# Kernel optimization log

Measured on AMD Instinct MI355X. Metric: run time of the kernel, lower is better.

Reference implementation:

```python
import jax, jax.numpy as jnp
import numpy as np

B, N, D = 256, 64, 256   # graphs, nodes/graph, hidden dim (node_size*extend_dim)
T, E = B * N, 524288     # total nodes, total edges
NODE, BOND, K = 128, 16, 3
RRELU_SLOPE = (1.0 / 8.0 + 1.0 / 3.0) / 2.0  # eval-mode RReLU slope


def rrelu(x):
    return jnp.where(x >= 0, x, RRELU_SLOPE * x)


def conv_step(x, src, dst, ea, Wn, We, bm, Ws, bs):
    # message on each edge, scatter-add to destination, self-transform + update
    msg = jax.nn.relu(x[src] @ Wn + ea @ We + bm)          # [E, D]
    agg = jax.ops.segment_sum(msg, dst, num_segments=T)    # [T, D]
    return jax.nn.relu(x @ Ws + agg + bs)


def readout(x):
    # GlobalPool: cat([mean, sum, sort_pool(k=3)], -1) -> [B, 5D]
    xr = x.reshape(B, N, D)
    mean, s = xr.mean(1), xr.sum(1)
    order = jnp.argsort(-xr[..., -1], axis=1)[:, :K]                      # [B, K]
    topk = jnp.take_along_axis(xr, order[..., None], axis=1).reshape(B, K * D)
    return jnp.concatenate([mean, s, topk], -1)


def dot_pool(x1, x2):
    # per-graph cross-molecule dot product, max & mean -> [B, 2]
    item = jnp.einsum('bnd,bmd->bnm', x1.reshape(B, N, D), x2.reshape(B, N, D))
    return jnp.stack([item.max((1, 2)), item.mean((1, 2))], -1)


def setup_inputs() -> dict:
    key = jax.random.key(0)
    ks = jax.random.split(key, 32)
    batch = jnp.repeat(jnp.arange(B, dtype=jnp.int64), N)
    off = jnp.repeat(jnp.arange(B, dtype=jnp.int64) * N, E // B)

    def edges(k):
        s = jax.random.randint(k, (2, E), 0, N).astype(jnp.int64) + off[None, :]
        return s

    def w(k, shape):
        fan = shape[0]
        return jax.random.normal(k, shape, jnp.float32) * (1.0 / np.sqrt(fan))

    return {
        'x1': jax.random.normal(ks[0], (T, NODE), jnp.float32),
        'edge_index1': edges(ks[1]),
        'edge_attr1': jax.random.normal(ks[2], (E, BOND), jnp.float32),
        'batch1': batch,
        'x2': jax.random.normal(ks[3], (T, NODE), jnp.float32),
        'edge_index2': edges(ks[4]),
        'edge_attr2': jax.random.normal(ks[5], (E, BOND), jnp.float32),
        'batch2': batch,
        'W0_1': w(ks[6], (NODE, D)), 'b0_1': jnp.zeros(D),
        'W0_2': w(ks[7], (NODE, D)), 'b0_2': jnp.zeros(D),
        'Wn1': w(ks[8], (D, D)), 'We1': w(ks[9], (BOND, D)), 'bm1': jnp.zeros(D),
        'Ws1': w(ks[10], (D, D)), 'bs1': jnp.zeros(D),
        'Wn2': w(ks[11], (D, D)), 'We2': w(ks[12], (BOND, D)), 'bm2': jnp.zeros(D),
        'Ws2': w(ks[13], (D, D)), 'bs2': jnp.zeros(D),
        'Wf1': w(ks[14], (5 * D, D)), 'bf1': jnp.zeros(D),
        'Wf2': w(ks[15], (5 * D, D)), 'bf2': jnp.zeros(D),
        'Wo1': w(ks[16], (2 * D + 6, D)), 'bo1': jnp.zeros(D),
        'Wo2': w(ks[17], (D, 2)), 'bo2': jnp.zeros(2),
    }


def reference(x1, edge_index1, edge_attr1, batch1, x2, edge_index2, edge_attr2, batch2,
              W0_1, b0_1, W0_2, b0_2,
              Wn1, We1, bm1, Ws1, bs1,
              Wn2, We2, bm2, Ws2, bs2,
              Wf1, bf1, Wf2, bf2, Wo1, bo1, Wo2, bo2):
    xm1 = rrelu(x1 @ W0_1 + b0_1)
    xm2 = rrelu(x2 @ W0_2 + b0_2)
    s1, d1 = edge_index1[0], edge_index1[1]
    s2, d2 = edge_index2[0], edge_index2[1]
    fusion = []
    for _ in range(3):  # message_steps
        xm1 = conv_step(xm1, s1, d1, edge_attr1, Wn1, We1, bm1, Ws1, bs1)
        xm2 = conv_step(xm2, s2, d2, edge_attr2, Wn2, We2, bm2, Ws2, bs2)
        fusion.append(dot_pool(xm1, xm2))
    outm1 = readout(xm1) @ Wf1 + bf1
    outm2 = readout(xm2) @ Wf2 + bf2
    out = jnp.concatenate([outm1, outm2, jnp.concatenate(fusion, -1)], -1)
    out = out @ Wo1 + bo1
    return out @ Wo2 + bo2
```

## Files before the change

kernel.cpp:

```cpp
#include <hip/hip_runtime.h>
#include <hip/hip_fp16.h>

#define E_TOTAL 524288
#define RRELU_SLOPE 0.22916666666666666f

typedef float f32x4 __attribute__((ext_vector_type(4)));
typedef short short8_t __attribute__((ext_vector_type(8)));
typedef _Float16 half4_t __attribute__((ext_vector_type(4)));
typedef _Float16 h2v __attribute__((ext_vector_type(2)));

#define MFMA16F16 __builtin_amdgcn_mfma_f32_16x16x16f16

#if defined(__HIP_DEVICE_COMPILE__)
# if __has_builtin(__builtin_amdgcn_cvt_pkrtz)
#  define HAVE_PKRTZ 1
# endif
#endif

__device__ inline unsigned short f2bf(float x) {
  unsigned int u = __float_as_uint(x);
  u += 0x7FFFu + ((u >> 16) & 1u);
  return (unsigned short)(u >> 16);
}

__device__ inline unsigned int pack_h2(float a, float b) {
  __half2 h = __floats2half2_rn(a, b);
  return __builtin_bit_cast(unsigned int, h);
}

__device__ inline unsigned int pack_h2_fast(float a, float b) {
#ifdef HAVE_PKRTZ
  return __builtin_bit_cast(unsigned int, __builtin_amdgcn_cvt_pkrtz(a, b));
#else
  return pack_h2(a, b);
#endif
}

__device__ inline float dot4(float4 a, float4 b) {
  return a.x * b.x + a.y * b.y + a.z * b.z + a.w * b.w;
}

__global__ __launch_bounds__(256) void gemm_bf16_dual(
    const float* __restrict__ A1, const unsigned short* __restrict__ BT1,
    const float* __restrict__ bias1, float* __restrict__ C1,
    const float* __restrict__ A2, const unsigned short* __restrict__ BT2,
    const float* __restrict__ bias2, float* __restrict__ C2,
    int lda, int ldc, int K, int act)
{
  const float* A = blockIdx.z ? A2 : A1;
  const unsigned short* BT = blockIdx.z ? BT2 : BT1;
  const float* bias = blockIdx.z ? bias2 : bias1;
  float* C = blockIdx.z ? C2 : C1;

  __shared__ unsigned short As[128][32];
  __shared__ unsigned short Bs[128][32];
  const int tid = threadIdx.x;
  const int bm = blockIdx.x, bn = blockIdx.y;
  const int w = tid >> 6, l = tid & 63;
  const int wm = (w & 1) * 64, wn = (w >> 1) * 64;
  const int q = l >> 4, r = l & 15;

  f32x4 acc[4][4];
  for (int i = 0; i < 4; ++i)
    for (int j = 0; j < 4; ++j)
      acc[i][j] = (f32x4){0.f, 0.f, 0.f, 0.f};

  const int sm = tid >> 1;
  const int sk = (tid & 1) * 16;
  const float* ap = A + (size_t)(bm * 128 + sm) * lda + sk;
  const unsigned short* bp = BT + (size_t)(bn * 128 + sm) * K + sk;

  for (int k0 = 0; k0 < K; k0 += 32) {
    float4 f0 = *(const float4*)(ap + k0);
    float4 f1 = *(const float4*)(ap + k0 + 4);
    float4 f2 = *(const float4*)(ap + k0 + 8);
    float4 f3 = *(const float4*)(ap + k0 + 12);
    uint4 p0, p1;
    p0.x = (unsigned)f2bf(f0.x) | ((unsigned)f2bf(f0.y) << 16);
    p0.y = (unsigned)f2bf(f0.z) | ((unsigned)f2bf(f0.w) << 16);
    p0.z = (unsigned)f2bf(f1.x) | ((unsigned)f2bf(f1.y) << 16);
    p0.w = (unsigned)f2bf(f1.z) | ((unsigned)f2bf(f1.w) << 16);
    p1.x = (unsigned)f2bf(f2.x) | ((unsigned)f2bf(f2.y) << 16);
    p1.y = (unsigned)f2bf(f2.z) | ((unsigned)f2bf(f2.w) << 16);
    p1.z = (unsigned)f2bf(f3.x) | ((unsigned)f2bf(f3.y) << 16);
    p1.w = (unsigned)f2bf(f3.z) | ((unsigned)f2bf(f3.w) << 16);
    *(uint4*)&As[sm][sk] = p0;
    *(uint4*)&As[sm][sk + 8] = p1;
    uint4 b0 = *(const uint4*)(bp + k0);
    uint4 b1 = *(const uint4*)(bp + k0 + 8);
    *(uint4*)&Bs[sm][sk] = b0;
    *(uint4*)&Bs[sm][sk + 8] = b1;
    __syncthreads();

    short8_t af[4], bfr[4];
    for (int mt = 0; mt < 4; ++mt)
      af[mt] = *(const short8_t*)&As[wm + mt * 16 + r][q * 8];
    for (int nt = 0; nt < 4; ++nt)
      bfr[nt] = *(const short8_t*)&Bs[wn + nt * 16 + r][q * 8];
    for (int mt = 0; mt < 4; ++mt)
      for (int nt = 0; nt < 4; ++nt)
        acc[mt][nt] = __builtin_amdgcn_mfma_f32_16x16x32_bf16(
            af[mt], bfr[nt], acc[mt][nt], 0, 0, 0);
    __syncthreads();
  }

  for (int nt = 0; nt < 4; ++nt) {
    int gc = bn * 128 + wn + nt * 16 + r;
    float bv = bias ? bias[gc] : 0.f;
    for (int mt = 0; mt < 4; ++mt) {
      int gm = bm * 128 + wm + mt * 16 + q * 4;
      for (int rr = 0; rr < 4; ++rr) {
        float v = acc[mt][nt][rr] + bv;
        if (act == 2) v = (v >= 0.f) ? v : v * RRELU_SLOPE;
        C[(size_t)(gm + rr) * ldc + gc] = v;
      }
    }
  }
}

__global__ __launch_bounds__(256) void sort_edges_dual(
    const int* __restrict__ ei1, const int* __restrict__ ei2,
    int* __restrict__ meta1, int* __restrict__ meta2,
    int* __restrict__ perm1, int* __restrict__ perm2,
    int* __restrict__ starts1, int* __restrict__ starts2)
{
  const int mol = blockIdx.x >> 8;
  const int g = blockIdx.x & 255;
  const int* eidx = mol ? ei2 : ei1;
  int* meta = mol ? meta2 : meta1;
  int* perm = mol ? perm2 : perm1;
  int* starts = mol ? starts2 : starts1;

  __shared__ int cnt[4][64];
  __shared__ int startS[65];
  __shared__ int cur[64];
  const int t = threadIdx.x, w = t >> 6;
  cnt[w][t & 63] = 0;
  if (t < 64) cur[t] = 0;
  __syncthreads();
  for (int i = t; i < 2048; i += 256)
    atomicAdd(&cnt[w][eidx[E_TOTAL + g * 2048 + i] & 63], 1);
  __syncthreads();
  if (t == 0) {
    int acc = 0;
    for (int n = 0; n < 64; ++n) {
      startS[n] = acc;
      acc += cnt[0][n] + cnt[1][n] + cnt[2][n] + cnt[3][n];
    }
    startS[64] = acc;
  }
  __syncthreads();
  if (t < 65) starts[g * 65 + t] = startS[t];
  for (int i = t; i < 2048; i += 256) {
    int s = eidx[g * 2048 + i] & 63;
    int d = eidx[E_TOTAL + g * 2048 + i] & 63;
    int p = startS[d] + atomicAdd(&cur[d], 1);
    meta[g * 2048 + p] = s | (d << 8);
    perm[g * 2048 + p] = i;
  }
}

__global__ __launch_bounds__(256) void ea_gather_pack_dual(
    const float* __restrict__ ea1, const float* __restrict__ ea2,
    const int* __restrict__ perm1, const int* __restrict__ perm2,
    unsigned int* __restrict__ o1, unsigned int* __restrict__ o2)
{
  const int mol = blockIdx.x >> 11;
  const float* ea = mol ? ea2 : ea1;
  const int* perm = mol ? perm2 : perm1;
  unsigned int* out = mol ? o2 : o1;
  int p = (blockIdx.x & 2047) * 256 + threadIdx.x;
  int g = p >> 11;
  int i = perm[p];
  const float* s = ea + (size_t)(g * 2048 + i) * 16;
  float4 v0 = *(const float4*)(s);
  float4 v1 = *(const float4*)(s + 4);
  float4 v2 = *(const float4*)(s + 8);
  float4 v3 = *(const float4*)(s + 12);
  uint4 q0, q1;
  q0.x = pack_h2(v0.x, v0.y); q0.y = pack_h2(v0.z, v0.w);
  q0.z = pack_h2(v1.x, v1.y); q0.w = pack_h2(v1.z, v1.w);
  q1.x = pack_h2(v2.x, v2.y); q1.y = pack_h2(v2.z, v2.w);
  q1.z = pack_h2(v3.x, v3.y); q1.w = pack_h2(v3.z, v3.w);
  *(uint4*)(out + (size_t)p * 8) = q0;
  *(uint4*)(out + (size_t)p * 8 + 4) = q1;
}

__global__ __launch_bounds__(512, 4) void edge_conv_dual(
    const float* __restrict__ y1, const int* __restrict__ meta1,
    const unsigned int* __restrict__ eas1, const unsigned int* __restrict__ wep1,
    const int* __restrict__ st1, float* __restrict__ xo1,
    const float* __restrict__ y2, const int* __restrict__ meta2,
    const unsigned int* __restrict__ eas2, const unsigned int* __restrict__ wep2,
    const int* __restrict__ st2, float* __restrict__ xo2)
{
  const float* y; const int* meta; const unsigned int* eas;
  const unsigned int* wep; const int* st; float* xo;
  if (blockIdx.z == 0) { y = y1; meta = meta1; eas = eas1; wep = wep1; st = st1; xo = xo1; }
  else                 { y = y2; meta = meta2; eas = eas2; wep = wep2; st = st2; xo = xo2; }

  __shared__ unsigned int ypk[4160];
  const int g = blockIdx.x >> 1;
  const int dbase = (blockIdx.x & 1) * 128;
  const int tid = threadIdx.x;
  const int l = tid & 63;
  const int w = tid >> 6;
  const int rh = l & 15;
  const int qh = l >> 4;
  const int rhw = w * 8 + rh;

  for (int i = tid; i < 4096; i += 512) {
    int n = i >> 6, j = i & 63;
    const float* yr = y + (size_t)(g * 64 + n) * 512 + dbase + j;
    ypk[n * 65 + j] = pack_h2_fast(yr[0], yr[64]);
  }

  uint2 bfr[8];
#pragma unroll
  for (int c = 0; c < 8; ++c) {
    int d = dbase + c * 16 + rh;
    bfr[c].x = wep[(2 * qh) * 256 + d];
    bfr[c].y = wep[(2 * qh + 1) * 256 + d];
  }

  __syncthreads();

  const int estart = st[g * 65 + w * 8];
  const int eend   = st[g * 65 + w * 8 + 8];

  f32x4 acc[8];
#pragma unroll
  for (int i = 0; i < 8; ++i) acc[i] = (f32x4){0.f, 0.f, 0.f, 0.f};

  int base = estart;
  uint2 af = {0u, 0u};
  int mv = -1;
  if (base < eend) {
    int lim = eend - base; if (lim > 16) lim = 16;
    af = *(const uint2*)(eas + ((size_t)g * 2048 + base + (rh < lim ? rh : lim - 1)) * 8 + 2 * qh);
    int m = meta[(size_t)g * 2048 + base + (l < lim ? l : lim - 1)];
    mv = (l < lim) ? m : -1;
  }

  while (base < eend) {
    int mp[4];
#pragma unroll
    for (int v = 0; v < 4; ++v)
      mp[v] = __builtin_amdgcn_ds_bpermute(qh * 16 + v * 4, mv);

    int nbase = base + 16;
    uint2 afn = af;
    int mvn = -1;
    if (nbase < eend) {
      int nlim = eend - nbase; if (nlim > 16) nlim = 16;
      afn = *(const uint2*)(eas + ((size_t)g * 2048 + nbase + (rh < nlim ? rh : nlim - 1)) * 8 + 2 * qh);
      int m2 = meta[(size_t)g * 2048 + nbase + (l < nlim ? l : nlim - 1)];
      mvn = (l < nlim) ? m2 : -1;
    }

    half4_t afh = __builtin_bit_cast(half4_t, af);
    f32x4 pa[4], pb[4];
#pragma unroll
    for (int cp = 0; cp < 4; ++cp) {
      f32x4 z = (f32x4){0.f, 0.f, 0.f, 0.f};
      pa[cp] = MFMA16F16(afh, __builtin_bit_cast(half4_t, bfr[cp]), z, 0, 0, 0);
      pb[cp] = MFMA16F16(afh, __builtin_bit_cast(half4_t, bfr[cp + 4]), z, 0, 0, 0);
    }

    unsigned int yv[4][4];
    unsigned int ind[4];
#pragma unroll
    for (int v = 0; v < 4; ++v) {
      int sv = mp[v] & 63;
      int dv = (mp[v] >> 8) & 255;
      const unsigned int* yb = ypk + sv * 65 + rh;
      yv[0][v] = yb[0];
      yv[1][v] = yb[16];
      yv[2][v] = yb[32];
      yv[3][v] = yb[48];
      ind[v] = (dv == rhw) ? 0x3C00u : 0u;
    }
    uint2 su;
    su.x = ind[0] | (ind[1] << 16);
    su.y = ind[2] | (ind[3] << 16);
    half4_t sfrag = __builtin_bit_cast(half4_t, su);

    const h2v hz = {(_Float16)0.0f, (_Float16)0.0f};
#pragma unroll
    for (int cp = 0; cp < 4; ++cp) {
      unsigned int t[4];
#pragma unroll
      for (int v = 0; v < 4; ++v) {
        h2v s = __builtin_bit_cast(h2v, pack_h2_fast(pa[cp][v], pb[cp][v]));
        s = s + __builtin_bit_cast(h2v, yv[cp][v]);
        s = __builtin_elementwise_max(s, hz);
        t[v] = __builtin_bit_cast(unsigned int, s);
      }
      uint2 blo, bhi;
      blo.x = __builtin_amdgcn_perm(t[1], t[0], 0x05040100u);
      blo.y = __builtin_amdgcn_perm(t[3], t[2], 0x05040100u);
      bhi.x = __builtin_amdgcn_perm(t[1], t[0], 0x07060302u);
      bhi.y = __builtin_amdgcn_perm(t[3], t[2], 0x07060302u);
      acc[cp]     = MFMA16F16(sfrag, __builtin_bit_cast(half4_t, blo), acc[cp], 0, 0, 0);
      acc[cp + 4] = MFMA16F16(sfrag, __builtin_bit_cast(half4_t, bhi), acc[cp + 4], 0, 0, 0);
    }

    base = nbase;
    af = afn;
    mv = mvn;
  }

  if (qh < 2) {
#pragma unroll
    for (int v = 0; v < 4; ++v) {
      int node = g * 64 + w * 8 + qh * 4 + v;
      const float* ysp = y + (size_t)node * 512 + 256 + dbase + rh;
      float* xop = xo + (size_t)node * 256 + dbase + rh;
#pragma unroll
      for (int cp = 0; cp < 8; ++cp) {
        int dim = (cp & 3) * 16 + (cp >> 2) * 64;
        xop[dim] = fmaxf(ysp[dim] + acc[cp][v], 0.f);
      }
    }
  }
}

__global__ __launch_bounds__(256) void dot_pool_k(
    const float* __restrict__ x1, const float* __restrict__ x2,
    float* __restrict__ fusion, int step)
{
  __shared__ float s1[64][68];
  __shared__ float s2[64][68];
  __shared__ float redm[4], reds[4];
  const int g = blockIdx.x;
  const int tid = threadIdx.x;
  const int ti = (tid & 15) * 4;
  const int tj = (tid >> 4) * 4;
  float acc[4][4] = {};
  for (int kc = 0; kc < 256; kc += 64) {
    for (int rr = 0; rr < 4; ++rr) {
      int lin = tid + rr * 256;
      int n = lin >> 4, k4 = (lin & 15) * 4;
      *(float4*)&s1[n][k4] = *(const float4*)(x1 + (size_t)(g * 64 + n) * 256 + kc + k4);
      *(float4*)&s2[n][k4] = *(const float4*)(x2 + (size_t)(g * 64 + n) * 256 + kc + k4);
    }
    __syncthreads();
    for (int kk = 0; kk < 64; kk += 4) {
      float4 a0 = *(const float4*)&s1[ti + 0][kk];
      float4 a1 = *(const float4*)&s1[ti + 1][kk];
      float4 a2 = *(const float4*)&s1[ti + 2][kk];
      float4 a3 = *(const float4*)&s1[ti + 3][kk];
      float4 b0 = *(const float4*)&s2[tj + 0][kk];
      float4 b1 = *(const float4*)&s2[tj + 1][kk];
      float4 b2 = *(const float4*)&s2[tj + 2][kk];
      float4 b3 = *(const float4*)&s2[tj + 3][kk];
      acc[0][0] += dot4(a0, b0); acc[0][1] += dot4(a0, b1);
      acc[0][2] += dot4(a0, b2); acc[0][3] += dot4(a0, b3);
      acc[1][0] += dot4(a1, b0); acc[1][1] += dot4(a1, b1);
      acc[1][2] += dot4(a1, b2); acc[1][3] += dot4(a1, b3);
      acc[2][0] += dot4(a2, b0); acc[2][1] += dot4(a2, b1);
      acc[2][2] += dot4(a2, b2); acc[2][3] += dot4(a2, b3);
      acc[3][0] += dot4(a3, b0); acc[3][1] += dot4(a3, b1);
      acc[3][2] += dot4(a3, b2); acc[3][3] += dot4(a3, b3);
    }
    __syncthreads();
  }
  float mymax = -1e30f, mysum = 0.f;
  for (int i = 0; i < 4; ++i)
    for (int j = 0; j < 4; ++j) {
      mymax = fmaxf(mymax, acc[i][j]);
      mysum += acc[i][j];
    }
  for (int off = 32; off; off >>= 1) {
    mymax = fmaxf(mymax, __shfl_down(mymax, off, 64));
    mysum += __shfl_down(mysum, off, 64);
  }
  if ((tid & 63) == 0) { redm[tid >> 6] = mymax; reds[tid >> 6] = mysum; }
  __syncthreads();
  if (tid == 0) {
    float gm = fmaxf(fmaxf(redm[0], redm[1]), fmaxf(redm[2], redm[3]));
    float gs = reds[0] + reds[1] + reds[2] + reds[3];
    fusion[g * 6 + step * 2] = gm;
    fusion[g * 6 + step * 2 + 1] = gs * (1.f / 4096.f);
  }
}

__global__ __launch_bounds__(256) void readout_dual(
    const float* __restrict__ xm1, const float* __restrict__ xm2,
    float* __restrict__ R1, float* __restrict__ R2)
{
  const int mol = blockIdx.x >> 8;
  const float* xm = mol ? xm2 : xm1;
  float* R = mol ? R2 : R1;
  __shared__ float lastcol[64];
  __shared__ int topi[3];
  const int g = blockIdx.x & 255, d = threadIdx.x;
  float s = 0.f;
  for (int n = 0; n < 64; ++n) s += xm[(size_t)(g * 64 + n) * 256 + d];
  R[(size_t)g * 1280 + d] = s * (1.f / 64.f);
  R[(size_t)g * 1280 + 256 + d] = s;
  if (d < 64) lastcol[d] = xm[(size_t)(g * 64 + d) * 256 + 255];
  __syncthreads();
  if (d == 0) {
    unsigned long long used = 0;
    for (int j = 0; j < 3; ++j) {
      float best = -1e30f;
      int bi = 0;
      for (int n = 0; n < 64; ++n) {
        if ((used >> n) & 1ull) continue;
        if (lastcol[n] > best) { best = lastcol[n]; bi = n; }
      }
      used |= (1ull << bi);
      topi[j] = bi;
    }
  }
  __syncthreads();
  for (int j = 0; j < 3; ++j)
    R[(size_t)g * 1280 + 512 + j * 256 + d] =
        xm[(size_t)(g * 64 + topi[j]) * 256 + d];
}

__global__ __launch_bounds__(256) void final_head(
    const float* __restrict__ outm1, const float* __restrict__ outm2,
    const float* __restrict__ fusion,
    const float* __restrict__ Wo1, const float* __restrict__ bo1,
    const float* __restrict__ Wo2, const float* __restrict__ bo2,
    float* __restrict__ out)
{
  __shared__ float cat[520];
  __shared__ float r0s[4], r1s[4];
  const int g = blockIdx.x, t = threadIdx.x;
  cat[t] = outm1[(size_t)g * 256 + t];
  cat[256 + t] = outm2[(size_t)g * 256 + t];
  if (t < 6) cat[512 + t] = fusion[g * 6 + t];
  __syncthreads();
  float a0 = 0.f, a1 = 0.f, a2 = 0.f, a3 = 0.f;
  for (int k = 0; k < 516; k += 4) {
    a0 = fmaf(cat[k],     Wo1[(size_t)(k)     * 256 + t], a0);
    a1 = fmaf(cat[k + 1], Wo1[(size_t)(k + 1) * 256 + t], a1);
    a2 = fmaf(cat[k + 2], Wo1[(size_t)(k + 2) * 256 + t], a2);
    a3 = fmaf(cat[k + 3], Wo1[(size_t)(k + 3) * 256 + t], a3);
  }
  a0 = fmaf(cat[516], Wo1[(size_t)516 * 256 + t], a0);
  a1 = fmaf(cat[517], Wo1[(size_t)517 * 256 + t], a1);
  float acc = bo1[t] + ((a0 + a1) + (a2 + a3));
  float p0 = acc * Wo2[t * 2];
  float p1 = acc * Wo2[t * 2 + 1];
  for (int off = 32; off; off >>= 1) {
    p0 += __shfl_down(p0, off, 64);
    p1 += __shfl_down(p1, off, 64);
  }
  if ((t & 63) == 0) { r0s[t >> 6] = p0; r1s[t >> 6] = p1; }
  __syncthreads();
  if (t == 0) {
    out[g * 2] = r0s[0] + r0s[1] + r0s[2] + r0s[3] + bo2[0];
    out[g * 2 + 1] = r1s[0] + r1s[1] + r1s[2] + r1s[3] + bo2[1];
  }
}

__global__ __launch_bounds__(256) void transpose_all(
    const float* __restrict__ W0_1, const float* __restrict__ W0_2,
    const float* __restrict__ Wn1, const float* __restrict__ Ws1,
    const float* __restrict__ Wn2, const float* __restrict__ Ws2,
    const float* __restrict__ Wf1, const float* __restrict__ Wf2,
    unsigned short* __restrict__ W0T1, unsigned short* __restrict__ W0T2,
    unsigned short* __restrict__ WcT1, unsigned short* __restrict__ WcT2,
    unsigned short* __restrict__ WfT1, unsigned short* __restrict__ WfT2)
{
  const int b = blockIdx.x, n = threadIdx.x;
  const float* src;
  unsigned short* dst;
  int k, K;
  if (b < 128)       { src = W0_1; dst = W0T1;        k = b;        K = 128; }
  else if (b < 256)  { src = W0_2; dst = W0T2;        k = b - 128;  K = 128; }
  else if (b < 512)  { src = Wn1;  dst = WcT1;        k = b - 256;  K = 256; }
  else if (b < 768)  { src = Ws1;  dst = WcT1 + 65536;k = b - 512;  K = 256; }
  else if (b < 1024) { src = Wn2;  dst = WcT2;        k = b - 768;  K = 256; }
  else if (b < 1280) { src = Ws2;  dst = WcT2 + 65536;k = b - 1024; K = 256; }
  else if (b < 2560) { src = Wf1;  dst = WfT1;        k = b - 1280; K = 1280; }
  else               { src = Wf2;  dst = WfT2;        k = b - 2560; K = 1280; }
  dst[n * K + k] = f2bf(src[(size_t)k * 256 + n]);
}

__global__ void misc_prep(
    const float* bm1, const float* bs1, const float* bm2, const float* bs2,
    const float* We1, const float* We2,
    float* bcat1, float* bcat2,
    unsigned int* weh1, unsigned int* weh2)
{
  int idx = blockIdx.x * 256 + threadIdx.x;
  if (idx < 512) {
    bcat1[idx] = idx < 256 ? bm1[idx] : bs1[idx - 256];
  } else if (idx < 1024) {
    int i = idx - 512;
    bcat2[i] = i < 256 ? bm2[i] : bs2[i - 256];
  } else if (idx < 3072) {
    int i = idx - 1024, j = i >> 8, d = i & 255;
    weh1[i] = pack_h2(We1[(2 * j) * 256 + d], We1[(2 * j + 1) * 256 + d]);
  } else if (idx < 5120) {
    int i = idx - 3072, j = i >> 8, d = i & 255;
    weh2[i] = pack_h2(We2[(2 * j) * 256 + d], We2[(2 * j + 1) * 256 + d]);
  }
}

extern "C" void kernel_launch(void* const* d_in, const int* in_sizes, int n_in,
                              void* d_out, int out_size, void* d_ws, size_t ws_size,
                              hipStream_t stream)
{
  const float* x1 = (const float*)d_in[0];
  const int* ei1 = (const int*)d_in[1];
  const float* ea1 = (const float*)d_in[2];
  const float* x2 = (const float*)d_in[4];
  const int* ei2 = (const int*)d_in[5];
  const float* ea2 = (const float*)d_in[6];
  const float* W0_1 = (const float*)d_in[8];
  const float* b0_1 = (const float*)d_in[9];
  const float* W0_2 = (const float*)d_in[10];
  const float* b0_2 = (const float*)d_in[11];
  const float* Wn1 = (const float*)d_in[12];
  const float* We1 = (const float*)d_in[13];
  const float* bm1 = (const float*)d_in[14];
  const float* Ws1 = (const float*)d_in[15];
  const float* bs1 = (const float*)d_in[16];
  const float* Wn2 = (const float*)d_in[17];
  const float* We2 = (const float*)d_in[18];
  const float* bm2 = (const float*)d_in[19];
  const float* Ws2 = (const float*)d_in[20];
  const float* bs2 = (const float*)d_in[21];
  const float* Wf1 = (const float*)d_in[22];
  const float* bf1 = (const float*)d_in[23];
  const float* Wf2 = (const float*)d_in[24];
  const float* bf2 = (const float*)d_in[25];
  const float* Wo1 = (const float*)d_in[26];
  const float* bo1 = (const float*)d_in[27];
  const float* Wo2 = (const float*)d_in[28];
  const float* bo2 = (const float*)d_in[29];
  float* out = (float*)d_out;

  float* w = (float*)d_ws;
  size_t off = 0;
  auto alloc = [&](size_t nf) { float* p = w + off; off += nf; return p; };
  float* xmA1 = alloc(4194304);
  float* xmA2 = alloc(4194304);
  float* xmB1 = alloc(4194304);
  float* xmB2 = alloc(4194304);
  float* y1 = alloc(8388608);
  float* y2 = alloc(8388608);
  float* R1 = alloc(327680);
  float* R2 = alloc(327680);
  float* outm1 = alloc(65536);
  float* outm2 = alloc(65536);
  float* fusion = alloc(1536);
  float* bcat1 = alloc(512);
  float* bcat2 = alloc(512);
  unsigned short* W0T1 = (unsigned short*)alloc(16384);
  unsigned short* W0T2 = (unsigned short*)alloc(16384);
  unsigned short* WcT1 = (unsigned short*)alloc(65536);
  unsigned short* WcT2 = (unsigned short*)alloc(65536);
  unsigned short* WfT1 = (unsigned short*)alloc(163840);
  unsigned short* WfT2 = (unsigned short*)alloc(163840);
  unsigned int* weh1 = (unsigned int*)alloc(2048);
  unsigned int* weh2 = (unsigned int*)alloc(2048);
  unsigned int* eah1 = (unsigned int*)alloc(4194304);
  unsigned int* eah2 = (unsigned int*)alloc(4194304);
  int* meta1 = (int*)alloc(524288);
  int* meta2 = (int*)alloc(524288);
  int* perm1 = (int*)alloc(524288);
  int* perm2 = (int*)alloc(524288);
  int* starts1 = (int*)alloc(16640);
  int* starts2 = (int*)alloc(16640);
  (void)in_sizes; (void)n_in; (void)out_size; (void)ws_size;

  sort_edges_dual<<<512, 256, 0, stream>>>(ei1, ei2, meta1, meta2,
                                           perm1, perm2, starts1, starts2);
  transpose_all<<<3840, 256, 0, stream>>>(W0_1, W0_2, Wn1, Ws1, Wn2, Ws2,
                                          Wf1, Wf2, W0T1, W0T2, WcT1, WcT2,
                                          WfT1, WfT2);
  misc_prep<<<20, 256, 0, stream>>>(bm1, bs1, bm2, bs2, We1, We2,
                                    bcat1, bcat2, weh1, weh2);
  ea_gather_pack_dual<<<4096, 256, 0, stream>>>(ea1, ea2, perm1, perm2,
                                                eah1, eah2);

  gemm_bf16_dual<<<dim3(128, 2, 2), 256, 0, stream>>>(
      x1, W0T1, b0_1, xmA1, x2, W0T2, b0_2, xmA2, 128, 256, 128, 2);

  float* cur1 = xmA1; float* cur2 = xmA2;
  float* nxt1 = xmB1; float* nxt2 = xmB2;
  for (int step = 0; step < 3; ++step) {
    gemm_bf16_dual<<<dim3(128, 4, 2), 256, 0, stream>>>(
        cur1, WcT1, bcat1, y1, cur2, WcT2, bcat2, y2, 256, 512, 256, 0);
    edge_conv_dual<<<dim3(512, 1, 2), 512, 0, stream>>>(
        y1, meta1, eah1, weh1, starts1, nxt1,
        y2, meta2, eah2, weh2, starts2, nxt2);
    dot_pool_k<<<256, 256, 0, stream>>>(nxt1, nxt2, fusion, step);
    float* t1 = cur1; cur1 = nxt1; nxt1 = t1;
    float* t2 = cur2; cur2 = nxt2; nxt2 = t2;
  }

  readout_dual<<<512, 256, 0, stream>>>(cur1, cur2, R1, R2);
  gemm_bf16_dual<<<dim3(2, 2, 2), 256, 0, stream>>>(
      R1, WfT1, bf1, outm1, R2, WfT2, bf2, outm2, 1280, 256, 1280, 0);
  final_head<<<256, 256, 0, stream>>>(outm1, outm2, fusion,
                                      Wo1, bo1, Wo2, bo2, out);
}
```

Measured before the change: 593.5 us.

## Emit bf16 node features for conv GEMM and MFMA dot-pool, tile weight transpose

The edge convolution and the initial projection now also write a bf16 copy of the node features. A new GEMM variant reads that bf16 copy directly instead of converting fp32 A tiles on load. The dot-pool kernel is rewritten to use bf16 MFMA with XOR-swizzled shared memory in place of the fp32 scalar dot products. The weight transpose now goes through a shared-memory tile with vectorized stores. This cuts A-operand bandwidth and moves dot-pool onto the matrix cores, at the cost of extra bf16 writes from edge_conv and lower precision in the dot-pool max and mean.

```diff
diff --git a/kernel.cpp b/kernel.cpp
--- a/kernel.cpp
+++ b/kernel.cpp
@@ -36,21 +36,20 @@
 #endif
 }
 
-__device__ inline float dot4(float4 a, float4 b) {
-  return a.x * b.x + a.y * b.y + a.z * b.z + a.w * b.w;
-}
-
 __global__ __launch_bounds__(256) void gemm_bf16_dual(
     const float* __restrict__ A1, const unsigned short* __restrict__ BT1,
     const float* __restrict__ bias1, float* __restrict__ C1,
+    unsigned short* __restrict__ Ch1,
     const float* __restrict__ A2, const unsigned short* __restrict__ BT2,
     const float* __restrict__ bias2, float* __restrict__ C2,
+    unsigned short* __restrict__ Ch2,
     int lda, int ldc, int K, int act)
 {
   const float* A = blockIdx.z ? A2 : A1;
   const unsigned short* BT = blockIdx.z ? BT2 : BT1;
   const float* bias = blockIdx.z ? bias2 : bias1;
   float* C = blockIdx.z ? C2 : C1;
+  unsigned short* Ch = blockIdx.z ? Ch2 : Ch1;
 
   __shared__ unsigned short As[128][32];
   __shared__ unsigned short Bs[128][32];
@@ -112,8 +111,73 @@
       for (int rr = 0; rr < 4; ++rr) {
         float v = acc[mt][nt][rr] + bv;
         if (act == 2) v = (v >= 0.f) ? v : v * RRELU_SLOPE;
-        C[(size_t)(gm + rr) * ldc + gc] = v;
+        if (Ch) Ch[(size_t)(gm + rr) * ldc + gc] = f2bf(v);
+        else    C[(size_t)(gm + rr) * ldc + gc] = v;
       }
+    }
+  }
+}
+
+__global__ __launch_bounds__(256) void gemm_h_dual(
+    const unsigned short* __restrict__ Ah1, const unsigned short* __restrict__ BT1,
+    const float* __restrict__ bias1, float* __restrict__ C1,
+    const unsigned short* __restrict__ Ah2, const unsigned short* __restrict__ BT2,
+    const float* __restrict__ bias2, float* __restrict__ C2,
+    int ldc, int K)
+{
+  const unsigned short* A = blockIdx.z ? Ah2 : Ah1;
+  const unsigned short* BT = blockIdx.z ? BT2 : BT1;
+  const float* bias = blockIdx.z ? bias2 : bias1;
+  float* C = blockIdx.z ? C2 : C1;
+
+  __shared__ unsigned short As[128][32];
+  __shared__ unsigned short Bs[128][32];
+  const int tid = threadIdx.x;
+  const int bm = blockIdx.x, bn = blockIdx.y;
+  const int w = tid >> 6, l = tid & 63;
+  const int wm = (w & 1) * 64, wn = (w >> 1) * 64;
+  const int q = l >> 4, r = l & 15;
+
+  f32x4 acc[4][4];
+  for (int i = 0; i < 4; ++i)
+    for (int j = 0; j < 4; ++j)
+      acc[i][j] = (f32x4){0.f, 0.f, 0.f, 0.f};
+
+  const int sm = tid >> 1;
+  const int sk = (tid & 1) * 16;
+  const unsigned short* ap = A + (size_t)(bm * 128 + sm) * K + sk;
+  const unsigned short* bp = BT + (size_t)(bn * 128 + sm) * K + sk;
+
+  for (int k0 = 0; k0 < K; k0 += 32) {
+    uint4 a0 = *(const uint4*)(ap + k0);
+    uint4 a1 = *(const uint4*)(ap + k0 + 8);
+    uint4 b0 = *(const uint4*)(bp + k0);
+    uint4 b1 = *(const uint4*)(bp + k0 + 8);
+    *(uint4*)&As[sm][sk] = a0;
+    *(uint4*)&As[sm][sk + 8] = a1;
+    *(uint4*)&Bs[sm][sk] = b0;
+    *(uint4*)&Bs[sm][sk + 8] = b1;
+    __syncthreads();
+
+    short8_t af[4], bfr[4];
+    for (int mt = 0; mt < 4; ++mt)
+      af[mt] = *(const short8_t*)&As[wm + mt * 16 + r][q * 8];
+    for (int nt = 0; nt < 4; ++nt)
+      bfr[nt] = *(const short8_t*)&Bs[wn + nt * 16 + r][q * 8];
+    for (int mt = 0; mt < 4; ++mt)
+      for (int nt = 0; nt < 4; ++nt)
+        acc[mt][nt] = __builtin_amdgcn_mfma_f32_16x16x32_bf16(
+            af[mt], bfr[nt], acc[mt][nt], 0, 0, 0);
+    __syncthreads();
+  }
+
+  for (int nt = 0; nt < 4; ++nt) {
+    int gc = bn * 128 + wn + nt * 16 + r;
+    float bv = bias ? bias[gc] : 0.f;
+    for (int mt = 0; mt < 4; ++mt) {
+      int gm = bm * 128 + wm + mt * 16 + q * 4;
+      for (int rr = 0; rr < 4; ++rr)
+        C[(size_t)(gm + rr) * ldc + gc] = acc[mt][nt][rr] + bv;
     }
   }
 }
@@ -190,14 +254,16 @@
     const float* __restrict__ y1, const int* __restrict__ meta1,
     const unsigned int* __restrict__ eas1, const unsigned int* __restrict__ wep1,
     const int* __restrict__ st1, float* __restrict__ xo1,
+    unsigned short* __restrict__ xoh1,
     const float* __restrict__ y2, const int* __restrict__ meta2,
     const unsigned int* __restrict__ eas2, const unsigned int* __restrict__ wep2,
-    const int* __restrict__ st2, float* __restrict__ xo2)
+    const int* __restrict__ st2, float* __restrict__ xo2,
+    unsigned short* __restrict__ xoh2)
 {
   const float* y; const int* meta; const unsigned int* eas;
-  const unsigned int* wep; const int* st; float* xo;
-  if (blockIdx.z == 0) { y = y1; meta = meta1; eas = eas1; wep = wep1; st = st1; xo = xo1; }
-  else                 { y = y2; meta = meta2; eas = eas2; wep = wep2; st = st2; xo = xo2; }
+  const unsigned int* wep; const int* st; float* xo; unsigned short* xoh;
+  if (blockIdx.z == 0) { y = y1; meta = meta1; eas = eas1; wep = wep1; st = st1; xo = xo1; xoh = xoh1; }
+  else                 { y = y2; meta = meta2; eas = eas2; wep = wep2; st = st2; xo = xo2; xoh = xoh2; }
 
   __shared__ unsigned int ypk[4160];
   const int g = blockIdx.x >> 1;
@@ -316,70 +382,73 @@
       int node = g * 64 + w * 8 + qh * 4 + v;
       const float* ysp = y + (size_t)node * 512 + 256 + dbase + rh;
       float* xop = xo + (size_t)node * 256 + dbase + rh;
+      unsigned short* xohp = xoh + (size_t)node * 256 + dbase + rh;
 #pragma unroll
       for (int cp = 0; cp < 8; ++cp) {
         int dim = (cp & 3) * 16 + (cp >> 2) * 64;
-        xop[dim] = fmaxf(ysp[dim] + acc[cp][v], 0.f);
+        float val = fmaxf(ysp[dim] + acc[cp][v], 0.f);
+        xop[dim] = val;
+        xohp[dim] = f2bf(val);
       }
     }
   }
 }
 
-__global__ __launch_bounds__(256) void dot_pool_k(
-    const float* __restrict__ x1, const float* __restrict__ x2,
+__global__ __launch_bounds__(256) void dot_pool_mfma(
+    const unsigned short* __restrict__ x1h, const unsigned short* __restrict__ x2h,
     float* __restrict__ fusion, int step)
 {
-  __shared__ float s1[64][68];
-  __shared__ float s2[64][68];
-  __shared__ float redm[4], reds[4];
-  const int g = blockIdx.x;
-  const int tid = threadIdx.x;
-  const int ti = (tid & 15) * 4;
-  const int tj = (tid >> 4) * 4;
-  float acc[4][4] = {};
-  for (int kc = 0; kc < 256; kc += 64) {
-    for (int rr = 0; rr < 4; ++rr) {
-      int lin = tid + rr * 256;
-      int n = lin >> 4, k4 = (lin & 15) * 4;
-      *(float4*)&s1[n][k4] = *(const float4*)(x1 + (size_t)(g * 64 + n) * 256 + kc + k4);
-      *(float4*)&s2[n][k4] = *(const float4*)(x2 + (size_t)(g * 64 + n) * 256 + kc + k4);
-    }
-    __syncthreads();
-    for (int kk = 0; kk < 64; kk += 4) {
-      float4 a0 = *(const float4*)&s1[ti + 0][kk];
-      float4 a1 = *(const float4*)&s1[ti + 1][kk];
-      float4 a2 = *(const float4*)&s1[ti + 2][kk];
-      float4 a3 = *(const float4*)&s1[ti + 3][kk];
-      float4 b0 = *(const float4*)&s2[tj + 0][kk];
-      float4 b1 = *(const float4*)&s2[tj + 1][kk];
-      float4 b2 = *(const float4*)&s2[tj + 2][kk];
-      float4 b3 = *(const float4*)&s2[tj + 3][kk];
-      acc[0][0] += dot4(a0, b0); acc[0][1] += dot4(a0, b1);
-      acc[0][2] += dot4(a0, b2); acc[0][3] += dot4(a0, b3);
-      acc[1][0] += dot4(a1, b0); acc[1][1] += dot4(a1, b1);
-      acc[1][2] += dot4(a1, b2); acc[1][3] += dot4(a1, b3);
-      acc[2][0] += dot4(a2, b0); acc[2][1] += dot4(a2, b1);
-      acc[2][2] += dot4(a2, b2); acc[2][3] += dot4(a2, b3);
-      acc[3][0] += dot4(a3, b0); acc[3][1] += dot4(a3, b1);
-      acc[3][2] += dot4(a3, b2); acc[3][3] += dot4(a3, b3);
-    }
-    __syncthreads();
-  }
+  __shared__ unsigned short s1[64][256];
+  __shared__ unsigned short s2[64][256];
+  const int g = blockIdx.x, tid = threadIdx.x;
+  const int l = tid & 63, w = tid >> 6;
+  const int r = l & 15, q = l >> 4;
+
+  for (int i = tid; i < 2048; i += 256) {
+    int row = i >> 5, c = i & 31;
+    int cs = c ^ (row & 7);
+    *(uint4*)&s1[row][cs * 8] = *(const uint4*)(x1h + (size_t)(g * 64 + row) * 256 + c * 8);
+    *(uint4*)&s2[row][cs * 8] = *(const uint4*)(x2h + (size_t)(g * 64 + row) * 256 + c * 8);
+  }
+  __syncthreads();
+
+  const int m0 = w * 16;
+  const int sx = r & 7;
+  f32x4 acc[4];
+#pragma unroll
+  for (int nt = 0; nt < 4; ++nt) acc[nt] = (f32x4){0.f, 0.f, 0.f, 0.f};
+
+#pragma unroll
+  for (int kb = 0; kb < 32; kb += 4) {
+    int ch = (kb + q) ^ sx;
+    short8_t af = *(const short8_t*)&s1[m0 + r][ch * 8];
+#pragma unroll
+    for (int nt = 0; nt < 4; ++nt) {
+      short8_t bf = *(const short8_t*)&s2[nt * 16 + r][ch * 8];
+      acc[nt] = __builtin_amdgcn_mfma_f32_16x16x32_bf16(af, bf, acc[nt], 0, 0, 0);
+    }
+  }
+
   float mymax = -1e30f, mysum = 0.f;
-  for (int i = 0; i < 4; ++i)
-    for (int j = 0; j < 4; ++j) {
-      mymax = fmaxf(mymax, acc[i][j]);
-      mysum += acc[i][j];
+#pragma unroll
+  for (int nt = 0; nt < 4; ++nt)
+#pragma unroll
+    for (int reg = 0; reg < 4; ++reg) {
+      float v = acc[nt][reg];
+      mymax = fmaxf(mymax, v);
+      mysum += v;
     }
   for (int off = 32; off; off >>= 1) {
     mymax = fmaxf(mymax, __shfl_down(mymax, off, 64));
     mysum += __shfl_down(mysum, off, 64);
   }
-  if ((tid & 63) == 0) { redm[tid >> 6] = mymax; reds[tid >> 6] = mysum; }
+  __syncthreads();
+  float* red = (float*)&s1[0][0];
+  if (l == 0) { red[w] = mymax; red[8 + w] = mysum; }
   __syncthreads();
   if (tid == 0) {
-    float gm = fmaxf(fmaxf(redm[0], redm[1]), fmaxf(redm[2], redm[3]));
-    float gs = reds[0] + reds[1] + reds[2] + reds[3];
+    float gm = fmaxf(fmaxf(red[0], red[1]), fmaxf(red[2], red[3]));
+    float gs = red[8] + red[9] + red[10] + red[11];
     fusion[g * 6 + step * 2] = gm;
     fusion[g * 6 + step * 2 + 1] = gs * (1.f / 4096.f);
   }
@@ -467,19 +536,33 @@
     unsigned short* __restrict__ WcT1, unsigned short* __restrict__ WcT2,
     unsigned short* __restrict__ WfT1, unsigned short* __restrict__ WfT2)
 {
-  const int b = blockIdx.x, n = threadIdx.x;
-  const float* src;
-  unsigned short* dst;
-  int k, K;
-  if (b < 128)       { src = W0_1; dst = W0T1;        k = b;        K = 128; }
-  else if (b < 256)  { src = W0_2; dst = W0T2;        k = b - 128;  K = 128; }
-  else if (b < 512)  { src = Wn1;  dst = WcT1;        k = b - 256;  K = 256; }
-  else if (b < 768)  { src = Ws1;  dst = WcT1 + 65536;k = b - 512;  K = 256; }
-  else if (b < 1024) { src = Wn2;  dst = WcT2;        k = b - 768;  K = 256; }
-  else if (b < 1280) { src = Ws2;  dst = WcT2 + 65536;k = b - 1024; K = 256; }
-  else if (b < 2560) { src = Wf1;  dst = WfT1;        k = b - 1280; K = 1280; }
-  else               { src = Wf2;  dst = WfT2;        k = b - 2560; K = 1280; }
-  dst[n * K + k] = f2bf(src[(size_t)k * 256 + n]);
+  const int b = blockIdx.x;
+  const float* src; unsigned short* dst; int k0, K;
+  if (b < 2)       { src = W0_1; dst = W0T1;         K = 128;  k0 = b * 64; }
+  else if (b < 4)  { src = W0_2; dst = W0T2;         K = 128;  k0 = (b - 2) * 64; }
+  else if (b < 8)  { src = Wn1;  dst = WcT1;         K = 256;  k0 = (b - 4) * 64; }
+  else if (b < 12) { src = Ws1;  dst = WcT1 + 65536; K = 256;  k0 = (b - 8) * 64; }
+  else if (b < 16) { src = Wn2;  dst = WcT2;         K = 256;  k0 = (b - 12) * 64; }
+  else if (b < 20) { src = Ws2;  dst = WcT2 + 65536; K = 256;  k0 = (b - 16) * 64; }
+  else if (b < 40) { src = Wf1;  dst = WfT1;         K = 1280; k0 = (b - 20) * 64; }
+  else             { src = Wf2;  dst = WfT2;         K = 1280; k0 = (b - 40) * 64; }
+
+  __shared__ unsigned short t[64][258];
+  const int tid = threadIdx.x;
+  for (int i = tid; i < 16384; i += 256) {
+    int row = i >> 8, col = i & 255;
+    t[row][col] = f2bf(src[(size_t)(k0 + row) * 256 + col]);
+  }
+  __syncthreads();
+  unsigned short* dp = dst + (size_t)tid * K + k0;
+  for (int k = 0; k < 64; k += 8) {
+    uint4 v;
+    v.x = (unsigned)t[k + 0][tid] | ((unsigned)t[k + 1][tid] << 16);
+    v.y = (unsigned)t[k + 2][tid] | ((unsigned)t[k + 3][tid] << 16);
+    v.z = (unsigned)t[k + 4][tid] | ((unsigned)t[k + 5][tid] << 16);
+    v.w = (unsigned)t[k + 6][tid] | ((unsigned)t[k + 7][tid] << 16);
+    *(uint4*)(dp + k) = v;
+  }
 }
 
 __global__ void misc_prep(
@@ -569,37 +652,47 @@
   int* perm2 = (int*)alloc(524288);
   int* starts1 = (int*)alloc(16640);
   int* starts2 = (int*)alloc(16640);
+  unsigned short* xmhA1 = (unsigned short*)alloc(2097152);
+  unsigned short* xmhA2 = (unsigned short*)alloc(2097152);
+  unsigned short* xmhB1 = (unsigned short*)alloc(2097152);
+  unsigned short* xmhB2 = (unsigned short*)alloc(2097152);
   (void)in_sizes; (void)n_in; (void)out_size; (void)ws_size;
 
   sort_edges_dual<<<512, 256, 0, stream>>>(ei1, ei2, meta1, meta2,
                                            perm1, perm2, starts1, starts2);
-  transpose_all<<<3840, 256, 0, stream>>>(W0_1, W0_2, Wn1, Ws1, Wn2, Ws2,
-                                          Wf1, Wf2, W0T1, W0T2, WcT1, WcT2,
-                                          WfT1, WfT2);
+  transpose_all<<<60, 256, 0, stream>>>(W0_1, W0_2, Wn1, Ws1, Wn2, Ws2,
+                                        Wf1, Wf2, W0T1, W0T2, WcT1, WcT2,
+                                        WfT1, WfT2);
   misc_prep<<<20, 256, 0, stream>>>(bm1, bs1, bm2, bs2, We1, We2,
                                     bcat1, bcat2, weh1, weh2);
   ea_gather_pack_dual<<<4096, 256, 0, stream>>>(ea1, ea2, perm1, perm2,
                                                 eah1, eah2);
 
   gemm_bf16_dual<<<dim3(128, 2, 2), 256, 0, stream>>>(
-      x1, W0T1, b0_1, xmA1, x2, W0T2, b0_2, xmA2, 128, 256, 128, 2);
+      x1, W0T1, b0_1, nullptr, xmhA1, x2, W0T2, b0_2, nullptr, xmhA2,
+      128, 256, 128, 2);
 
   float* cur1 = xmA1; float* cur2 = xmA2;
   float* nxt1 = xmB1; float* nxt2 = xmB2;
+  unsigned short* curh1 = xmhA1; unsigned short* curh2 = xmhA2;
+  unsigned short* nxth1 = xmhB1; unsigned short* nxth2 = xmhB2;
   for (int step = 0; step < 3; ++step) {
-    gemm_bf16_dual<<<dim3(128, 4, 2), 256, 0, stream>>>(
-        cur1, WcT1, bcat1, y1, cur2, WcT2, bcat2, y2, 256, 512, 256, 0);
+    gemm_h_dual<<<dim3(128, 4, 2), 256, 0, stream>>>(
+        curh1, WcT1, bcat1, y1, curh2, WcT2, bcat2, y2, 512, 256);
     edge_conv_dual<<<dim3(512, 1, 2), 512, 0, stream>>>(
-        y1, meta1, eah1, weh1, starts1, nxt1,
-        y2, meta2, eah2, weh2, starts2, nxt2);
-    dot_pool_k<<<256, 256, 0, stream>>>(nxt1, nxt2, fusion, step);
+        y1, meta1, eah1, weh1, starts1, nxt1, nxth1,
+        y2, meta2, eah2, weh2, starts2, nxt2, nxth2);
+    dot_pool_mfma<<<256, 256, 0, stream>>>(nxth1, nxth2, fusion, step);
     float* t1 = cur1; cur1 = nxt1; nxt1 = t1;
     float* t2 = cur2; cur2 = nxt2; nxt2 = t2;
+    unsigned short* th1 = curh1; curh1 = nxth1; nxth1 = th1;
+    unsigned short* th2 = curh2; curh2 = nxth2; nxth2 = th2;
   }
 
   readout_dual<<<512, 256, 0, stream>>>(cur1, cur2, R1, R2);
   gemm_bf16_dual<<<dim3(2, 2, 2), 256, 0, stream>>>(
-      R1, WfT1, bf1, outm1, R2, WfT2, bf2, outm2, 1280, 256, 1280, 0);
+      R1, WfT1, bf1, outm1, nullptr, R2, WfT2, bf2, outm2, nullptr,
+      1280, 256, 1280, 0);
   final_head<<<256, 256, 0, stream>>>(outm1, outm2, fusion,
                                       Wo1, bo1, Wo2, bo2, out);
 }
```

Result: faster. 544.6 us (-8.2%).
